# Optimization experiments

Hardware: AMD Instinct MI355X
Metric: run time of the kernel (lower is better)

Reference implementation:

```python
import jax, jax.numpy as jnp
import numpy as np

N = 100000
E = 800000
D_IN, D_H, D_OUT = 128, 128, 128


def setup_inputs() -> dict:
    key = jax.random.key(0)
    ks = jax.random.split(key, 8)
    x = jax.random.normal(ks[0], (N, D_IN), dtype=jnp.float32)
    edge_index = jax.random.randint(ks[1], (2, E), 0, N, dtype=jnp.int64)
    s = 1.0 / np.sqrt(D_IN)
    W1 = jax.random.uniform(ks[2], (D_H, D_IN), minval=-s, maxval=s, dtype=jnp.float32)
    b1 = jax.random.uniform(ks[3], (D_H,), minval=-s, maxval=s, dtype=jnp.float32)
    sh = 1.0 / np.sqrt(D_H)
    W2 = jax.random.uniform(ks[4], (D_H, D_H), minval=-sh, maxval=sh, dtype=jnp.float32)
    b2 = jax.random.uniform(ks[5], (D_H,), minval=-sh, maxval=sh, dtype=jnp.float32)
    W3 = jax.random.uniform(ks[6], (D_OUT, D_H), minval=-sh, maxval=sh, dtype=jnp.float32)
    b3 = jax.random.uniform(ks[7], (D_OUT,), minval=-sh, maxval=sh, dtype=jnp.float32)
    return {"x": x, "edge_index": edge_index, "W1": W1, "b1": b1,
            "W2": W2, "b2": b2, "W3": W3, "b3": b3}


def reference(x, edge_index, W1, b1, W2, b2, W3, b3):
    row, col = edge_index[0], edge_index[1]
    n = x.shape[0]
    # in-degree of destination nodes (bincount over row), clamped to 1
    deg = jnp.clip(
        jax.ops.segment_sum(jnp.ones_like(row, dtype=x.dtype), row, num_segments=n),
        1.0)  # [N]

    def mp(h):
        # gather messages from source nodes, scatter-add to destinations, mean, relu
        agg = jax.ops.segment_sum(h[col], row, num_segments=n)  # [N, d]
        return jax.nn.relu(agg / deg[:, None])

    h = mp(x @ W1.T + b1)
    h = mp(h @ W2.T + b2)
    return h @ W3.T + b3
```

## Files before the change

### kernel.cpp

```cpp
#include <hip/hip_runtime.h>

#define NNODES 100000
#define NEDGES 800000
#define D 128
#define NB1 391


__global__ __launch_bounds__(256) void k_count(const int* __restrict__ ei,
                                               int* __restrict__ cnt) {
    int e = blockIdx.x * 256 + threadIdx.x;
    atomicAdd(&cnt[ei[e]], 1);
}

__global__ __launch_bounds__(256) void k_scan1(const int* __restrict__ cnt,
                                               int* __restrict__ off,
                                               int* __restrict__ bsum) {
    __shared__ int s[256];
    int t = threadIdx.x;
    int i = blockIdx.x * 256 + t;
    int v = (i < NNODES) ? cnt[i] : 0;
    s[t] = v;
    __syncthreads();
    for (int d = 1; d < 256; d <<= 1) {
        int a = (t >= d) ? s[t - d] : 0;
        __syncthreads();
        s[t] += a;
        __syncthreads();
    }
    if (i < NNODES) off[i] = s[t] - v;
    if (t == 255) bsum[blockIdx.x] = s[255];
}

__global__ __launch_bounds__(512) void k_scan2(int* __restrict__ bsum) {
    __shared__ int s[512];
    int t = threadIdx.x;
    int v = (t < NB1) ? bsum[t] : 0;
    s[t] = v;
    __syncthreads();
    for (int d = 1; d < 512; d <<= 1) {
        int a = (t >= d) ? s[t - d] : 0;
        __syncthreads();
        s[t] += a;
        __syncthreads();
    }
    if (t < NB1) bsum[t] = s[t] - v;
}

__global__ __launch_bounds__(256) void k_scan3(int* __restrict__ off,
                                               const int* __restrict__ bsum,
                                               int* __restrict__ cur) {
    int i = blockIdx.x * 256 + threadIdx.x;
    if (i < NNODES) {
        int o = off[i] + bsum[blockIdx.x];
        off[i] = o;
        cur[i] = o;
    }
}

__global__ __launch_bounds__(256) void k_fill(const int* __restrict__ ei,
                                              int* __restrict__ cur,
                                              int* __restrict__ csr) {
    int e = blockIdx.x * 256 + threadIdx.x;
    int r = ei[e];
    int c = ei[NEDGES + e];
    int p = atomicAdd(&cur[r], 1);
    csr[p] = c;
}


__global__ __launch_bounds__(256) void k_tr(const float* __restrict__ W,
                                            float* __restrict__ Wt) {
    int i = blockIdx.x * 256 + threadIdx.x;
    int j = i >> 7, k = i & 127;
    Wt[k * D + j] = W[i];
}


static __device__ __forceinline__ void fma4(float4& acc, float s, const float4& v) {
    acc.x = fmaf(s, v.x, acc.x);
    acc.y = fmaf(s, v.y, acc.y);
    acc.z = fmaf(s, v.z, acc.z);
    acc.w = fmaf(s, v.w, acc.w);
}

__global__ __launch_bounds__(512, 6) void k_gemm(const float* __restrict__ in,
                                                 const float* __restrict__ Wt,
                                                 const float* __restrict__ bias,
                                                 float* __restrict__ out) {
    __shared__ float Ws[D * 64];
    int t = threadIdx.x;
    int bh = blockIdx.x & 1;
    int nblk = blockIdx.x >> 1;
    const float4* Wg = (const float4*)Wt;
#pragma unroll
    for (int it = 0; it < 4; ++it) {
        int i4 = it * 512 + t;
        int k = i4 >> 4, cg = i4 & 15;
        ((float4*)Ws)[i4] = Wg[k * 32 + bh * 16 + cg];
    }
    int jl = t & 15;
    int ng = t >> 4;
    int j0 = jl * 4;
    float4 b4 = *(const float4*)(bias + bh * 64 + j0);
    __syncthreads();

    int nb = nblk * 128 + ng * 4;
    if (nb >= NNODES) return;
    const float* p0 = in + (size_t)(nb + 0) * D;
    const float* p1 = in + (size_t)(nb + 1) * D;
    const float* p2 = in + (size_t)(nb + 2) * D;
    const float* p3 = in + (size_t)(nb + 3) * D;
    float4 a0 = b4, a1 = b4, a2 = b4, a3 = b4;
#pragma unroll 4
    for (int k = 0; k < D; k += 4) {
        const float4 w0 = *(const float4*)(Ws + (k + 0) * 64 + j0);
        const float4 w1 = *(const float4*)(Ws + (k + 1) * 64 + j0);
        const float4 w2 = *(const float4*)(Ws + (k + 2) * 64 + j0);
        const float4 w3 = *(const float4*)(Ws + (k + 3) * 64 + j0);
        float4 x0 = *(const float4*)(p0 + k);
        float4 x1 = *(const float4*)(p1 + k);
        float4 x2 = *(const float4*)(p2 + k);
        float4 x3 = *(const float4*)(p3 + k);
        fma4(a0, x0.x, w0); fma4(a0, x0.y, w1); fma4(a0, x0.z, w2); fma4(a0, x0.w, w3);
        fma4(a1, x1.x, w0); fma4(a1, x1.y, w1); fma4(a1, x1.z, w2); fma4(a1, x1.w, w3);
        fma4(a2, x2.x, w0); fma4(a2, x2.y, w1); fma4(a2, x2.z, w2); fma4(a2, x2.w, w3);
        fma4(a3, x3.x, w0); fma4(a3, x3.y, w1); fma4(a3, x3.z, w2); fma4(a3, x3.w, w3);
    }
    int jo = bh * 64 + j0;
    *(float4*)(out + (size_t)(nb + 0) * D + jo) = a0;
    *(float4*)(out + (size_t)(nb + 1) * D + jo) = a1;
    *(float4*)(out + (size_t)(nb + 2) * D + jo) = a2;
    *(float4*)(out + (size_t)(nb + 3) * D + jo) = a3;
}


__global__ __launch_bounds__(256) void k_mp(const float* __restrict__ h,
                                            const int* __restrict__ off,
                                            const int* __restrict__ cnt,
                                            const int* __restrict__ csr,
                                            float* __restrict__ agg) {
    int gid = blockIdx.x * 256 + threadIdx.x;
    int node = gid >> 6;
    int lane = threadIdx.x & 63;
    if (node >= NNODES) return;
    int b = off[node];
    int c = cnt[node];
    float ax = 0.f, ay = 0.f;
    int e = 0;
    for (; e + 8 <= c; e += 8) {
        int s0 = csr[b + e + 0];
        int s1 = csr[b + e + 1];
        int s2 = csr[b + e + 2];
        int s3 = csr[b + e + 3];
        int s4 = csr[b + e + 4];
        int s5 = csr[b + e + 5];
        int s6 = csr[b + e + 6];
        int s7 = csr[b + e + 7];
        float2 v0 = *(const float2*)(h + (size_t)s0 * D + lane * 2);
        float2 v1 = *(const float2*)(h + (size_t)s1 * D + lane * 2);
        float2 v2 = *(const float2*)(h + (size_t)s2 * D + lane * 2);
        float2 v3 = *(const float2*)(h + (size_t)s3 * D + lane * 2);
        float2 v4 = *(const float2*)(h + (size_t)s4 * D + lane * 2);
        float2 v5 = *(const float2*)(h + (size_t)s5 * D + lane * 2);
        float2 v6 = *(const float2*)(h + (size_t)s6 * D + lane * 2);
        float2 v7 = *(const float2*)(h + (size_t)s7 * D + lane * 2);
        ax += ((v0.x + v1.x) + (v2.x + v3.x)) + ((v4.x + v5.x) + (v6.x + v7.x));
        ay += ((v0.y + v1.y) + (v2.y + v3.y)) + ((v4.y + v5.y) + (v6.y + v7.y));
    }
    for (; e + 4 <= c; e += 4) {
        int s0 = csr[b + e + 0];
        int s1 = csr[b + e + 1];
        int s2 = csr[b + e + 2];
        int s3 = csr[b + e + 3];
        float2 v0 = *(const float2*)(h + (size_t)s0 * D + lane * 2);
        float2 v1 = *(const float2*)(h + (size_t)s1 * D + lane * 2);
        float2 v2 = *(const float2*)(h + (size_t)s2 * D + lane * 2);
        float2 v3 = *(const float2*)(h + (size_t)s3 * D + lane * 2);
        ax += (v0.x + v1.x) + (v2.x + v3.x);
        ay += (v0.y + v1.y) + (v2.y + v3.y);
    }
    for (; e < c; ++e) {
        int s = csr[b + e];
        float2 v = *(const float2*)(h + (size_t)s * D + lane * 2);
        ax += v.x;
        ay += v.y;
    }
    float inv = 1.0f / fmaxf((float)c, 1.0f);
    float2 r;
    r.x = fmaxf(ax * inv, 0.f);
    r.y = fmaxf(ay * inv, 0.f);
    *(float2*)(agg + (size_t)node * D + lane * 2) = r;
}


extern "C" void kernel_launch(void* const* d_in, const int* in_sizes, int n_in,
                              void* d_out, int out_size, void* d_ws, size_t ws_size,
                              hipStream_t stream) {
    const float* x  = (const float*)d_in[0];
    const int*   ei = (const int*)d_in[1];
    const float* W1 = (const float*)d_in[2];
    const float* b1 = (const float*)d_in[3];
    const float* W2 = (const float*)d_in[4];
    const float* b2 = (const float*)d_in[5];
    const float* W3 = (const float*)d_in[6];
    const float* b3 = (const float*)d_in[7];
    float* out = (float*)d_out;

    char* ws = (char*)d_ws;
    int* cnt  = (int*)(ws + 0);
    int* off  = (int*)(ws + (512 << 10));
    int* cur  = (int*)(ws + (1024 << 10));
    int* bsum = (int*)(ws + (1536 << 10));
    int* csr  = (int*)(ws + (2 << 20));
    float* Wt1 = (float*)(ws + ((size_t)6 << 20));
    float* Wt2 = (float*)(ws + ((size_t)6 << 20) + 65536);
    float* Wt3 = (float*)(ws + ((size_t)6 << 20) + 131072);
    float* A  = (float*)(ws + ((size_t)8 << 20));
    float* B  = (float*)(ws + ((size_t)64 << 20));

    hipMemsetAsync(cnt, 0, NNODES * sizeof(int), stream);
    k_tr<<<64, 256, 0, stream>>>(W1, Wt1);
    k_tr<<<64, 256, 0, stream>>>(W2, Wt2);
    k_tr<<<64, 256, 0, stream>>>(W3, Wt3);
    k_count<<<NEDGES / 256, 256, 0, stream>>>(ei, cnt);
    k_scan1<<<NB1, 256, 0, stream>>>(cnt, off, bsum);
    k_scan2<<<1, 512, 0, stream>>>(bsum);
    k_scan3<<<NB1, 256, 0, stream>>>(off, bsum, cur);
    k_fill<<<NEDGES / 256, 256, 0, stream>>>(ei, cur, csr);

    int gemmGrid = 2 * ((NNODES + 127) / 128);
    k_gemm<<<gemmGrid, 512, 0, stream>>>(x, Wt1, b1, A);
    k_mp<<<NNODES / 4, 256, 0, stream>>>(A, off, cnt, csr, B);
    k_gemm<<<gemmGrid, 512, 0, stream>>>(B, Wt2, b2, out);
    k_mp<<<NNODES / 4, 256, 0, stream>>>(out, off, cnt, csr, A);
    k_gemm<<<gemmGrid, 512, 0, stream>>>(A, Wt3, b3, out);
}
```

Measured before the change: 506.2 us.

## Enlarge GEMM row tile to 8 with double-buffered loads; fuse transposes

The GEMM kernel now computes 8 rows per thread instead of 4, with register double-buffering of the input loads across k-steps, and the grid is halved to match. Launch bounds drop from 6 to 4 waves to leave room for the extra registers. The three weight-transpose launches are merged into one kernel, and the message-passing kernel reads offset and count through readfirstlane so they become scalar values. The changes target GEMM load latency, redundant shared-memory weight reads and launch overhead, at the cost of higher register pressure and lower occupancy.

```diff
diff --git a/kernel.cpp b/kernel.cpp
--- a/kernel.cpp
+++ b/kernel.cpp
@@ -68,11 +68,18 @@
 }
 
 
-__global__ __launch_bounds__(256) void k_tr(const float* __restrict__ W,
-                                            float* __restrict__ Wt) {
-    int i = blockIdx.x * 256 + threadIdx.x;
+__global__ __launch_bounds__(256) void k_tr3(const float* __restrict__ W1,
+                                             const float* __restrict__ W2,
+                                             const float* __restrict__ W3,
+                                             float* __restrict__ T1,
+                                             float* __restrict__ T2,
+                                             float* __restrict__ T3) {
+    int bb = blockIdx.x;
+    const float* W = (bb < 64) ? W1 : (bb < 128) ? W2 : W3;
+    float* T = (bb < 64) ? T1 : (bb < 128) ? T2 : T3;
+    int i = (bb & 63) * 256 + threadIdx.x;
     int j = i >> 7, k = i & 127;
-    Wt[k * D + j] = W[i];
+    T[k * D + j] = W[i];
 }
 
 
@@ -83,7 +90,7 @@
     acc.w = fmaf(s, v.w, acc.w);
 }
 
-__global__ __launch_bounds__(512, 6) void k_gemm(const float* __restrict__ in,
+__global__ __launch_bounds__(512, 4) void k_gemm(const float* __restrict__ in,
                                                  const float* __restrict__ Wt,
                                                  const float* __restrict__ bias,
                                                  float* __restrict__ out) {
@@ -104,33 +111,49 @@
     float4 b4 = *(const float4*)(bias + bh * 64 + j0);
     __syncthreads();
 
-    int nb = nblk * 128 + ng * 4;
+    int nb = nblk * 256 + ng * 8;
     if (nb >= NNODES) return;
-    const float* p0 = in + (size_t)(nb + 0) * D;
-    const float* p1 = in + (size_t)(nb + 1) * D;
-    const float* p2 = in + (size_t)(nb + 2) * D;
-    const float* p3 = in + (size_t)(nb + 3) * D;
-    float4 a0 = b4, a1 = b4, a2 = b4, a3 = b4;
-#pragma unroll 4
-    for (int k = 0; k < D; k += 4) {
-        const float4 w0 = *(const float4*)(Ws + (k + 0) * 64 + j0);
-        const float4 w1 = *(const float4*)(Ws + (k + 1) * 64 + j0);
-        const float4 w2 = *(const float4*)(Ws + (k + 2) * 64 + j0);
-        const float4 w3 = *(const float4*)(Ws + (k + 3) * 64 + j0);
-        float4 x0 = *(const float4*)(p0 + k);
-        float4 x1 = *(const float4*)(p1 + k);
-        float4 x2 = *(const float4*)(p2 + k);
-        float4 x3 = *(const float4*)(p3 + k);
-        fma4(a0, x0.x, w0); fma4(a0, x0.y, w1); fma4(a0, x0.z, w2); fma4(a0, x0.w, w3);
-        fma4(a1, x1.x, w0); fma4(a1, x1.y, w1); fma4(a1, x1.z, w2); fma4(a1, x1.w, w3);
-        fma4(a2, x2.x, w0); fma4(a2, x2.y, w1); fma4(a2, x2.z, w2); fma4(a2, x2.w, w3);
-        fma4(a3, x3.x, w0); fma4(a3, x3.y, w1); fma4(a3, x3.z, w2); fma4(a3, x3.w, w3);
-    }
+    const float* p = in + (size_t)nb * D;
+
+    float4 acc[8];
+#pragma unroll
+    for (int r = 0; r < 8; ++r) acc[r] = b4;
+    float4 xa[8], xb[8];
+
+    auto loadx = [&](float4* buf, int kk) {
+#pragma unroll
+        for (int r = 0; r < 8; ++r) buf[r] = *(const float4*)(p + r * D + kk);
+    };
+    auto fmall = [&](const float4* buf, int kk) {
+        const float4 w0 = *(const float4*)(Ws + (kk + 0) * 64 + j0);
+        const float4 w1 = *(const float4*)(Ws + (kk + 1) * 64 + j0);
+        const float4 w2 = *(const float4*)(Ws + (kk + 2) * 64 + j0);
+        const float4 w3 = *(const float4*)(Ws + (kk + 3) * 64 + j0);
+#pragma unroll
+        for (int r = 0; r < 8; ++r) {
+            fma4(acc[r], buf[r].x, w0);
+            fma4(acc[r], buf[r].y, w1);
+            fma4(acc[r], buf[r].z, w2);
+            fma4(acc[r], buf[r].w, w3);
+        }
+    };
+
+    loadx(xa, 0);
+#pragma unroll 1
+    for (int k = 0; k < D - 8; k += 8) {
+        loadx(xb, k + 4);
+        fmall(xa, k);
+        loadx(xa, k + 8);
+        fmall(xb, k + 4);
+    }
+    loadx(xb, D - 4);
+    fmall(xa, D - 8);
+    fmall(xb, D - 4);
+
     int jo = bh * 64 + j0;
-    *(float4*)(out + (size_t)(nb + 0) * D + jo) = a0;
-    *(float4*)(out + (size_t)(nb + 1) * D + jo) = a1;
-    *(float4*)(out + (size_t)(nb + 2) * D + jo) = a2;
-    *(float4*)(out + (size_t)(nb + 3) * D + jo) = a3;
+    float* o = out + (size_t)nb * D + jo;
+#pragma unroll
+    for (int r = 0; r < 8; ++r) *(float4*)(o + r * D) = acc[r];
 }
 
 
@@ -143,8 +166,8 @@
     int node = gid >> 6;
     int lane = threadIdx.x & 63;
     if (node >= NNODES) return;
-    int b = off[node];
-    int c = cnt[node];
+    int b = __builtin_amdgcn_readfirstlane(off[node]);
+    int c = __builtin_amdgcn_readfirstlane(cnt[node]);
     float ax = 0.f, ay = 0.f;
     int e = 0;
     for (; e + 8 <= c; e += 8) {
@@ -219,16 +242,14 @@
     float* B  = (float*)(ws + ((size_t)64 << 20));
 
     hipMemsetAsync(cnt, 0, NNODES * sizeof(int), stream);
-    k_tr<<<64, 256, 0, stream>>>(W1, Wt1);
-    k_tr<<<64, 256, 0, stream>>>(W2, Wt2);
-    k_tr<<<64, 256, 0, stream>>>(W3, Wt3);
+    k_tr3<<<192, 256, 0, stream>>>(W1, W2, W3, Wt1, Wt2, Wt3);
     k_count<<<NEDGES / 256, 256, 0, stream>>>(ei, cnt);
     k_scan1<<<NB1, 256, 0, stream>>>(cnt, off, bsum);
     k_scan2<<<1, 512, 0, stream>>>(bsum);
     k_scan3<<<NB1, 256, 0, stream>>>(off, bsum, cur);
     k_fill<<<NEDGES / 256, 256, 0, stream>>>(ei, cur, csr);
 
-    int gemmGrid = 2 * ((NNODES + 127) / 128);
+    int gemmGrid = 2 * ((NNODES + 255) / 256);
     k_gemm<<<gemmGrid, 512, 0, stream>>>(x, Wt1, b1, A);
     k_mp<<<NNODES / 4, 256, 0, stream>>>(A, off, cnt, csr, B);
     k_gemm<<<gemmGrid, 512, 0, stream>>>(B, Wt2, b2, out);
```

New measurement: 531.8 us. 1.05x slower.
